# Kernel tuning notes

Hardware: AMD Instinct MI355X
Metric: run time of the kernel (lower is better)

## Reference

```python
import jax, jax.numpy as jnp
import numpy as np
from jax import lax

B, L, DIN, H = 16, 100, 6144, 1024
DI, N, DTR, K, NC = 2048, 16, 64, 4, 16  # d_inner, d_state, dt_rank, d_conv, num_classes


def setup_inputs() -> dict:
    key = jax.random.key(0)
    ks = jax.random.split(key, 10)
    def s(k, shape, sc=0.02):
        return jax.random.normal(k, shape, dtype=jnp.float32) * sc
    return dict(
        x=jax.random.normal(ks[0], (B, L, DIN), dtype=jnp.float32),
        W_in=s(ks[1], (DIN, H)), b_in=jnp.zeros((H,), jnp.float32),
        in_proj_w=s(ks[2], (H, 2 * DI)),
        conv_w=s(ks[3], (DI, K), 0.1), conv_b=jnp.zeros((DI,), jnp.float32),
        x_proj_w=s(ks[4], (DI, DTR + 2 * N)),
        dt_proj_w=s(ks[5], (DTR, DI), 0.1),
        dt_proj_b=jnp.full((DI,), float(np.log(np.expm1(0.01))), jnp.float32),
        A_log=jnp.log(jnp.broadcast_to(jnp.arange(1, N + 1, dtype=jnp.float32), (DI, N))),
        D=jnp.ones((DI,), jnp.float32),
        out_proj_w=s(ks[6], (DI, H)),
        W_out=s(ks[7], (H, NC)), b_out=jnp.zeros((NC,), jnp.float32),
    )


def reference(x, W_in, b_in, in_proj_w, conv_w, conv_b, x_proj_w,
              dt_proj_w, dt_proj_b, A_log, D, out_proj_w, W_out, b_out):
    # input projection: [B,L,DIN] -> [B,L,H]
    h = x @ W_in + b_in
    # Mamba block
    xz = h @ in_proj_w                      # [B,L,2*DI]
    xm, z = xz[..., :DI], xz[..., DI:]
    # depthwise causal conv1d, kernel K
    xp = jnp.pad(xm, ((0, 0), (K - 1, 0), (0, 0)))
    xc = sum(conv_w[:, k] * xp[:, k:k + L, :] for k in range(K)) + conv_b
    xc = jax.nn.silu(xc)                    # [B,L,DI]
    # input-dependent dt, B, C
    proj = xc @ x_proj_w                    # [B,L,DTR+2N]
    dt = proj[..., :DTR]
    Bm = proj[..., DTR:DTR + N]             # [B,L,N]
    Cm = proj[..., DTR + N:]                # [B,L,N]
    delta = jax.nn.softplus(dt @ dt_proj_w + dt_proj_b)  # [B,L,DI]
    A = -jnp.exp(A_log)                     # [DI,N]
    dA = jnp.exp(jnp.einsum('bld,dn->bldn', delta, A))          # [B,L,DI,N]
    dBx = (delta * xc)[..., None] * Bm[:, :, None, :]            # [B,L,DI,N]
    # selective scan over time: h_t = dA_t * h_{t-1} + dBx_t
    def step(hprev, inp):
        dA_t, dBx_t = inp
        hnew = dA_t * hprev + dBx_t
        return hnew, hnew
    h0 = jnp.zeros((xm.shape[0], DI, N), xm.dtype)
    _, hs = lax.scan(step, h0, (dA.transpose(1, 0, 2, 3), dBx.transpose(1, 0, 2, 3)))
    y = jnp.einsum('lbdn,bln->bld', hs, Cm)  # [B,L,DI]
    y = y + D * xc
    y = y * jax.nn.silu(z)
    out = y @ out_proj_w                     # [B,L,H]
    logits = out @ W_out + b_out             # [B,L,NC]
    return logits
```

## Files before the change

### kernel.cpp

```cpp
#include <hip/hip_runtime.h>
#include <hip/hip_bf16.h>
#include <stdint.h>

constexpr int Bb  = 16;
constexpr int Ll  = 100;
constexpr int DIN = 6144;
constexpr int Hh  = 1024;
constexpr int DI  = 2048;
constexpr int Nst = 16;
constexpr int DTR = 64;
constexpr int Kc  = 4;
constexpr int NC  = 16;
constexpr int M   = Bb * Ll;
constexpr int NCH = 4;
constexpr int CL  = Ll / NCH;

typedef __attribute__((ext_vector_type(8))) short short8;
typedef __attribute__((ext_vector_type(4))) float floatx4;

__device__ __forceinline__ float bf2f(unsigned short u) {
    union { uint32_t b; float f; } x; x.b = ((uint32_t)u) << 16; return x.f;
}
__device__ __forceinline__ unsigned short f2bf(float f) {
    union { float f; uint32_t b; } x; x.f = f;
    uint32_t r = x.b + 0x7FFF + ((x.b >> 16) & 1);
    return (unsigned short)(r >> 16);
}
__device__ __forceinline__ float fast_silu(float x) {
    return x / (1.f + __expf(-x));
}


template<bool SPLIT, bool BIAS, bool W16>
__global__ __launch_bounds__(512) void gemm_deep(
    const unsigned short* __restrict__ A, int lda,
    const unsigned short* __restrict__ Bt, int ldb,
    const float* __restrict__ bias,
    unsigned short* __restrict__ C16,
    unsigned short* __restrict__ Cpart,
    int Md, int Nd, int Kslab)
{
    __shared__ short As[3 * 256 * 64];
    __shared__ short Bs[3 * 128 * 64];

    const int nx = gridDim.x, ny = gridDim.y, nz = gridDim.z;
    const int nb = nx * ny * nz;
    int id = blockIdx.x + nx * (blockIdx.y + ny * blockIdx.z);
    int bx, by, bz;
    if ((nb & 7) == 0) {
        int swz = (id & 7) * (nb >> 3) + (id >> 3);
        bx = swz % nx;
        int rem = swz / nx;
        by = rem % ny;
        bz = rem / ny;
    } else {
        bx = blockIdx.x; by = blockIdx.y; bz = blockIdx.z;
    }

    const int tid  = threadIdx.x;
    const int lane = tid & 63;
    const int wid  = tid >> 6;
    const int wr   = wid >> 1;
    const int wc   = wid & 1;
    const int l15  = lane & 15;
    const int kg   = lane >> 4;
    const int gsw  = l15 & 7;
    const int m0   = bx * 256;
    const int n0   = by * 128;
    const int kbeg = SPLIT ? bz * Kslab : 0;

    floatx4 acc[4][4];
    #pragma unroll
    for (int m = 0; m < 4; m++)
        #pragma unroll
        for (int n = 0; n < 4; n++)
            acc[m][n] = (floatx4){0.f, 0.f, 0.f, 0.f};

    auto stage = [&](int buf, int k0) {
        #pragma unroll
        for (int j = 0; j < 4; j++) {
            int c = j * 512 + tid;
            int row = c >> 3, gl = c & 7;
            int gg = gl ^ (row & 7);
            int grow = m0 + row; grow = grow < Md ? grow : Md - 1;
            const __attribute__((address_space(1))) short* src =
                (const __attribute__((address_space(1))) short*)(A + (size_t)grow * lda + k0 + gg * 8);
            __builtin_amdgcn_global_load_lds(
                (const __attribute__((address_space(1))) void*)src,
                (__attribute__((address_space(3))) void*)&As[(buf * 2048 + c) * 8], 16, 0, 0);
        }
        #pragma unroll
        for (int j = 0; j < 2; j++) {
            int c = j * 512 + tid;
            int row = c >> 3, gl = c & 7;
            int gg = gl ^ (row & 7);
            int brow = n0 + row; brow = brow < Nd ? brow : Nd - 1;
            const __attribute__((address_space(1))) short* src =
                (const __attribute__((address_space(1))) short*)(Bt + (size_t)brow * ldb + k0 + gg * 8);
            __builtin_amdgcn_global_load_lds(
                (const __attribute__((address_space(1))) void*)src,
                (__attribute__((address_space(3))) void*)&Bs[(buf * 1024 + c) * 8], 16, 0, 0);
        }
    };

    const int nt = Kslab >> 6;
    stage(0, kbeg);
    stage(1, kbeg + 64);

    for (int t = 0; t < nt; t++) {
        const int cur = t % 3;
        if (t + 2 < nt) {
            stage((t + 2) % 3, kbeg + (t + 2) * 64);
            asm volatile("s_waitcnt vmcnt(12)" ::: "memory");
        } else if (t + 1 < nt) {
            asm volatile("s_waitcnt vmcnt(6)" ::: "memory");
        } else {
            asm volatile("s_waitcnt vmcnt(0)" ::: "memory");
        }
        __builtin_amdgcn_s_barrier();
        __builtin_amdgcn_sched_barrier(0);

        short8 a[2][4], bfr[2][4];
        #pragma unroll
        for (int kk = 0; kk < 2; kk++) {
            #pragma unroll
            for (int m = 0; m < 4; m++) {
                int row = wr * 64 + m * 16 + l15;
                int gs  = (kk * 4 + kg) ^ gsw;
                a[kk][m] = *(const short8*)&As[(cur * 2048 + row * 8 + gs) * 8];
            }
            #pragma unroll
            for (int n = 0; n < 4; n++) {
                int row = wc * 64 + n * 16 + l15;
                int gs  = (kk * 4 + kg) ^ gsw;
                bfr[kk][n] = *(const short8*)&Bs[(cur * 1024 + row * 8 + gs) * 8];
            }
        }
        __builtin_amdgcn_s_setprio(1);
        #pragma unroll
        for (int kk = 0; kk < 2; kk++)
            #pragma unroll
            for (int m = 0; m < 4; m++)
                #pragma unroll
                for (int n = 0; n < 4; n++)
                    acc[m][n] = __builtin_amdgcn_mfma_f32_16x16x32_bf16(a[kk][m], bfr[kk][n], acc[m][n], 0, 0, 0);
        __builtin_amdgcn_s_setprio(0);
        __builtin_amdgcn_sched_barrier(0);
        __builtin_amdgcn_s_barrier();
    }

    unsigned short* Cs = (unsigned short*)As;
    #pragma unroll
    for (int n = 0; n < 4; n++) {
        int col = wc * 64 + n * 16 + l15;
        float bv = BIAS ? bias[n0 + col] : 0.f;
        #pragma unroll
        for (int m = 0; m < 4; m++) {
            #pragma unroll
            for (int q = 0; q < 4; q++) {
                int row = wr * 64 + m * 16 + kg * 4 + q;
                Cs[row * 136 + col] = f2bf(acc[m][n][q] + bv);
            }
        }
    }
    __syncthreads();
    #pragma unroll
    for (int j = 0; j < 8; j++) {
        int c = j * 512 + tid;
        int row = c >> 4, cc = c & 15;
        int grow = m0 + row;
        if (grow >= Md) continue;
        short8 v = *(const short8*)&Cs[row * 136 + cc * 8];
        if (SPLIT)
            *(short8*)&Cpart[(size_t)bz * Md * Nd + (size_t)grow * Nd + n0 + cc * 8] = v;
        else if (W16)
            *(short8*)&C16[(size_t)grow * Nd + n0 + cc * 8] = v;
    }
}

template<bool SPLIT, bool PARTBF, bool BIAS, int ACT, bool W32, bool W16>
__global__ __launch_bounds__(256) void gemm_mfma(
    const unsigned short* __restrict__ A, int lda,
    const unsigned short* __restrict__ Bt, int ldb,
    const float* __restrict__ bias,
    float* __restrict__ C32,
    unsigned short* __restrict__ C16,
    void* __restrict__ Cpart,
    int Md, int Nd, int Kslab)
{
    __shared__ short As[2][128 * 64];
    __shared__ short Bs[2][128 * 64];

    const int nx = gridDim.x, ny = gridDim.y, nz = gridDim.z;
    const int nb = nx * ny * nz;
    int id = blockIdx.x + nx * (blockIdx.y + ny * blockIdx.z);
    int bx, by, bz;
    if ((nb & 7) == 0) {
        int swz = (id & 7) * (nb >> 3) + (id >> 3);
        bx = swz % nx;
        int rem = swz / nx;
        by = rem % ny;
        bz = rem / ny;
    } else {
        bx = blockIdx.x; by = blockIdx.y; bz = blockIdx.z;
    }

    const int tid  = threadIdx.x;
    const int lane = tid & 63;
    const int wid  = tid >> 6;
    const int wr   = wid >> 1;
    const int wc   = wid & 1;
    const int l15  = lane & 15;
    const int kg   = lane >> 4;
    const int gsw  = l15 & 7;
    const int m0   = bx * 128;
    const int n0   = by * 128;
    const int kbeg = SPLIT ? bz * Kslab : 0;

    floatx4 acc[4][4];
    #pragma unroll
    for (int m = 0; m < 4; m++)
        #pragma unroll
        for (int n = 0; n < 4; n++)
            acc[m][n] = (floatx4){0.f, 0.f, 0.f, 0.f};

    auto stage = [&](int buf, int k0) {
        #pragma unroll
        for (int j = 0; j < 4; j++) {
            int c = j * 256 + tid;
            int row = c >> 3, gl = c & 7;
            int gg = gl ^ (row & 7);
            int grow = m0 + row; grow = grow < Md ? grow : Md - 1;
            const __attribute__((address_space(1))) short* src =
                (const __attribute__((address_space(1))) short*)(A + (size_t)grow * lda + k0 + gg * 8);
            __builtin_amdgcn_global_load_lds(
                (const __attribute__((address_space(1))) void*)src,
                (__attribute__((address_space(3))) void*)&As[buf][c * 8], 16, 0, 0);
        }
        #pragma unroll
        for (int j = 0; j < 4; j++) {
            int c = j * 256 + tid;
            int row = c >> 3, gl = c & 7;
            int gg = gl ^ (row & 7);
            int brow = n0 + row; brow = brow < Nd ? brow : Nd - 1;
            const __attribute__((address_space(1))) short* src =
                (const __attribute__((address_space(1))) short*)(Bt + (size_t)brow * ldb + k0 + gg * 8);
            __builtin_amdgcn_global_load_lds(
                (const __attribute__((address_space(1))) void*)src,
                (__attribute__((address_space(3))) void*)&Bs[buf][c * 8], 16, 0, 0);
        }
    };

    stage(0, kbeg);
    asm volatile("s_waitcnt vmcnt(0)" ::: "memory");
    __builtin_amdgcn_s_barrier();
    __builtin_amdgcn_sched_barrier(0);

    const int nt = Kslab >> 6;
    for (int t = 0; t < nt; t++) {
        const int cur = t & 1;
        if (t + 1 < nt) {
            stage(cur ^ 1, kbeg + (t + 1) * 64);
            asm volatile("s_waitcnt vmcnt(8)" ::: "memory");
        } else {
            asm volatile("s_waitcnt vmcnt(0)" ::: "memory");
        }
        __builtin_amdgcn_s_barrier();
        __builtin_amdgcn_sched_barrier(0);

        short8 a[2][4], bfr[2][4];
        #pragma unroll
        for (int kk = 0; kk < 2; kk++) {
            #pragma unroll
            for (int m = 0; m < 4; m++) {
                int row = wr * 64 + m * 16 + l15;
                int gs  = (kk * 4 + kg) ^ gsw;
                a[kk][m] = *(const short8*)&As[cur][(row * 8 + gs) * 8];
            }
            #pragma unroll
            for (int n = 0; n < 4; n++) {
                int row = wc * 64 + n * 16 + l15;
                int gs  = (kk * 4 + kg) ^ gsw;
                bfr[kk][n] = *(const short8*)&Bs[cur][(row * 8 + gs) * 8];
            }
        }
        #pragma unroll
        for (int kk = 0; kk < 2; kk++)
            #pragma unroll
            for (int m = 0; m < 4; m++)
                #pragma unroll
                for (int n = 0; n < 4; n++)
                    acc[m][n] = __builtin_amdgcn_mfma_f32_16x16x32_bf16(a[kk][m], bfr[kk][n], acc[m][n], 0, 0, 0);

        __builtin_amdgcn_sched_barrier(0);
        __builtin_amdgcn_s_barrier();
    }

    if (SPLIT) {
        #pragma unroll
        for (int n = 0; n < 4; n++) {
            int col = n0 + wc * 64 + n * 16 + l15;
            if (col >= Nd) continue;
            #pragma unroll
            for (int m = 0; m < 4; m++)
                #pragma unroll
                for (int q = 0; q < 4; q++) {
                    int row = m0 + wr * 64 + m * 16 + kg * 4 + q;
                    if (row >= Md) continue;
                    size_t ix = (size_t)bz * Md * Nd + (size_t)row * Nd + col;
                    if (PARTBF) ((unsigned short*)Cpart)[ix] = f2bf(acc[m][n][q]);
                    else        ((float*)Cpart)[ix] = acc[m][n][q];
                }
        }
    } else {
        #pragma unroll
        for (int n = 0; n < 4; n++) {
            int col = n0 + wc * 64 + n * 16 + l15;
            if (col >= Nd) continue;
            float bv = BIAS ? bias[col] : 0.f;
            #pragma unroll
            for (int m = 0; m < 4; m++)
                #pragma unroll
                for (int q = 0; q < 4; q++) {
                    int row = m0 + wr * 64 + m * 16 + kg * 4 + q;
                    if (row >= Md) continue;
                    float v = acc[m][n][q] + bv;
                    if (ACT == 1) v = fmaxf(v, 0.f) + log1pf(expf(-fabsf(v)));
                    if (W32) C32[(size_t)row * Nd + col] = v;
                    if (W16) C16[(size_t)row * Nd + col] = f2bf(v);
                }
        }
    }
}

template<int S, bool BIAS, int ACT, bool W32, bool W16>
__global__ __launch_bounds__(256) void reduce_split(
    const float* __restrict__ P, const float* __restrict__ bias,
    float* __restrict__ C32, unsigned short* __restrict__ C16,
    int total, int nmask)
{
    int i = (blockIdx.x * 256 + threadIdx.x) * 4;
    float4 v = *(const float4*)&P[i];
    #pragma unroll
    for (int s = 1; s < S; s++) {
        float4 p = *(const float4*)&P[(size_t)s * total + i];
        v.x += p.x; v.y += p.y; v.z += p.z; v.w += p.w;
    }
    float r[4] = {v.x, v.y, v.z, v.w};
    #pragma unroll
    for (int j = 0; j < 4; j++) {
        float t = r[j];
        if (BIAS) t += bias[(i + j) & nmask];
        if (ACT == 1) t = fmaxf(t, 0.f) + log1pf(expf(-fabsf(t)));
        if (W32) C32[i + j] = t;
        if (W16) C16[i + j] = f2bf(t);
    }
}

template<int S, bool BIAS>
__global__ __launch_bounds__(256) void reduce_split_bf(
    const unsigned short* __restrict__ P, const float* __restrict__ bias,
    unsigned short* __restrict__ C16, int total, int nmask)
{
    int i = (blockIdx.x * 256 + threadIdx.x) * 8;
    float r[8] = {};
    #pragma unroll
    for (int s = 0; s < S; s++) {
        short8 p = *(const short8*)&P[(size_t)s * total + i];
        #pragma unroll
        for (int j = 0; j < 8; j++) r[j] += bf2f((unsigned short)p[j]);
    }
    short8 o;
    #pragma unroll
    for (int j = 0; j < 8; j++) {
        float t = r[j];
        if (BIAS) t += bias[(i + j) & nmask];
        o[j] = (short)f2bf(t);
    }
    *(short8*)&C16[i] = o;
}

__global__ __launch_bounds__(256) void f32_to_bf16_kernel(
    const float* __restrict__ in, unsigned short* __restrict__ out, int n4)
{
    int i = (blockIdx.x * 256 + threadIdx.x) * 4;
    float4 v = *(const float4*)&in[i];
    out[i + 0] = f2bf(v.x);
    out[i + 1] = f2bf(v.y);
    out[i + 2] = f2bf(v.z);
    out[i + 3] = f2bf(v.w);
}

__global__ __launch_bounds__(256) void transpose_f32_bf16(
    const float* __restrict__ in, unsigned short* __restrict__ out, int K, int N)
{
    __shared__ float t[32][33];
    int k0 = blockIdx.x * 32, n0 = blockIdx.y * 32;
    int tx = threadIdx.x & 31, ty = threadIdx.x >> 5;
    #pragma unroll
    for (int i = 0; i < 4; i++)
        t[ty + i * 8][tx] = in[(size_t)(k0 + ty + i * 8) * N + n0 + tx];
    __syncthreads();
    #pragma unroll
    for (int i = 0; i < 4; i++)
        out[(size_t)(n0 + ty + i * 8) * K + k0 + tx] = f2bf(t[tx][ty + i * 8]);
}

__global__ __launch_bounds__(256) void conv_silu_kernel(
    const unsigned short* __restrict__ xz, const float* __restrict__ conv_w,
    const float* __restrict__ conv_b, float* __restrict__ xc,
    unsigned short* __restrict__ xc_bf)
{
    int idx = blockIdx.x * 256 + threadIdx.x;
    if (idx >= Bb * Ll * DI) return;
    int d  = idx & (DI - 1);
    int bl = idx >> 11;
    int l  = bl % Ll;

    float acc = conv_b[d];
    #pragma unroll
    for (int k = 0; k < Kc; k++) {
        int ls = l + k - (Kc - 1);
        if (ls >= 0)
            acc = fmaf(conv_w[d * Kc + k], bf2f(xz[(size_t)(bl + ls - l) * (2 * DI) + d]), acc);
    }
    float s = fast_silu(acc);
    xc[idx] = s;
    xc_bf[idx] = f2bf(s);
}

__global__ __launch_bounds__(256) void scan_part1(
    const float* __restrict__ delta, const float* __restrict__ xc,
    const float* __restrict__ proj,  const float* __restrict__ A_log,
    float* __restrict__ Pbuf, float* __restrict__ Sbuf)
{
    const int t    = threadIdx.x;
    const int nq   = t & 3;
    const int dloc = t >> 2;
    const int d    = blockIdx.x * 64 + dloc;
    const int b    = blockIdx.y;
    const int c    = blockIdx.z;

    float4 Alq = *(const float4*)&A_log[(size_t)d * Nst + nq * 4];
    float Ar0 = -expf(Alq.x), Ar1 = -expf(Alq.y), Ar2 = -expf(Alq.z), Ar3 = -expf(Alq.w);

    float h0 = 0.f, h1 = 0.f, h2 = 0.f, h3 = 0.f;
    float sdl = 0.f;

    for (int l = c * CL; l < (c + 1) * CL; l++) {
        size_t bl = (size_t)b * Ll + l;
        float dl  = delta[bl * DI + d];
        float xcv = xc[bl * DI + d];
        float dx  = dl * xcv;
        float4 Bv = *(const float4*)&proj[bl * (DTR + 2 * Nst) + DTR + nq * 4];

        h0 = fmaf(__expf(dl * Ar0), h0, dx * Bv.x);
        h1 = fmaf(__expf(dl * Ar1), h1, dx * Bv.y);
        h2 = fmaf(__expf(dl * Ar2), h2, dx * Bv.z);
        h3 = fmaf(__expf(dl * Ar3), h3, dx * Bv.w);
        sdl += dl;
    }

    size_t o = (((size_t)c * Bb + b) * DI + d) * Nst + nq * 4;
    *(float4*)&Pbuf[o] = (float4){__expf(sdl * Ar0), __expf(sdl * Ar1),
                                  __expf(sdl * Ar2), __expf(sdl * Ar3)};
    *(float4*)&Sbuf[o] = (float4){h0, h1, h2, h3};
}

__global__ __launch_bounds__(256) void scan_part2(
    const float* __restrict__ delta, const float* __restrict__ xc,
    const unsigned short* __restrict__ xz, const float* __restrict__ proj,
    const float* __restrict__ A_log, const float* __restrict__ Dv,
    const float* __restrict__ Pbuf, const float* __restrict__ Sbuf,
    unsigned short* __restrict__ y)
{
    const int t    = threadIdx.x;
    const int nq   = t & 3;
    const int dloc = t >> 2;
    const int d    = blockIdx.x * 64 + dloc;
    const int b    = blockIdx.y;
    const int c    = blockIdx.z;

    float4 Alq = *(const float4*)&A_log[(size_t)d * Nst + nq * 4];
    float Ar0 = -expf(Alq.x), Ar1 = -expf(Alq.y), Ar2 = -expf(Alq.z), Ar3 = -expf(Alq.w);
    const float Dd = Dv[d];

    float h0 = 0.f, h1 = 0.f, h2 = 0.f, h3 = 0.f;
    for (int cc = 0; cc < c; cc++) {
        size_t o = (((size_t)cc * Bb + b) * DI + d) * Nst + nq * 4;
        float4 Pv = *(const float4*)&Pbuf[o];
        float4 Sv = *(const float4*)&Sbuf[o];
        h0 = fmaf(Pv.x, h0, Sv.x);
        h1 = fmaf(Pv.y, h1, Sv.y);
        h2 = fmaf(Pv.z, h2, Sv.z);
        h3 = fmaf(Pv.w, h3, Sv.w);
    }

    for (int l = c * CL; l < (c + 1) * CL; l++) {
        size_t bl = (size_t)b * Ll + l;
        float dl  = delta[bl * DI + d];
        float xcv = xc[bl * DI + d];
        float zv  = bf2f(xz[bl * (2 * DI) + DI + d]);
        float dx  = dl * xcv;
        const float* p = proj + bl * (DTR + 2 * Nst);
        float4 Bv = *(const float4*)&p[DTR + nq * 4];
        float4 Cv = *(const float4*)&p[DTR + Nst + nq * 4];

        h0 = fmaf(__expf(dl * Ar0), h0, dx * Bv.x);
        h1 = fmaf(__expf(dl * Ar1), h1, dx * Bv.y);
        h2 = fmaf(__expf(dl * Ar2), h2, dx * Bv.z);
        h3 = fmaf(__expf(dl * Ar3), h3, dx * Bv.w);

        float yac = h0 * Cv.x + h1 * Cv.y + h2 * Cv.z + h3 * Cv.w;
        yac += __shfl_xor(yac, 1);
        yac += __shfl_xor(yac, 2);

        if (nq == 0) {
            float yv = yac + Dd * xcv;
            yv *= fast_silu(zv);
            y[bl * DI + d] = f2bf(yv);
        }
    }
}

__global__ __launch_bounds__(256) void gemm_n16(
    const unsigned short* __restrict__ A, const float* __restrict__ W,
    const float* __restrict__ bias, float* __restrict__ C, int Kd)
{
    int m  = blockIdx.x;
    int t  = threadIdx.x;
    int c  = t & 15;
    int kg = t >> 4;
    const unsigned short* a = A + (size_t)m * Kd;

    float acc = 0.f;
    for (int k = kg; k < Kd; k += 16)
        acc = fmaf(bf2f(a[k]), W[k * NC + c], acc);

    __shared__ float red[256];
    red[t] = acc;
    __syncthreads();
    #pragma unroll
    for (int s = 128; s >= 16; s >>= 1) {
        if (t < s) red[t] += red[t + s];
        __syncthreads();
    }
    if (t < 16) C[(size_t)m * NC + t] = red[t] + bias[t];
}

extern "C" void kernel_launch(void* const* d_in, const int* in_sizes, int n_in,
                              void* d_out, int out_size, void* d_ws, size_t ws_size,
                              hipStream_t stream) {
    const float* x         = (const float*)d_in[0];
    const float* W_in      = (const float*)d_in[1];
    const float* b_in      = (const float*)d_in[2];
    const float* in_proj_w = (const float*)d_in[3];
    const float* conv_w    = (const float*)d_in[4];
    const float* conv_b    = (const float*)d_in[5];
    const float* x_proj_w  = (const float*)d_in[6];
    const float* dt_proj_w = (const float*)d_in[7];
    const float* dt_proj_b = (const float*)d_in[8];
    const float* A_log     = (const float*)d_in[9];
    const float* Dv        = (const float*)d_in[10];
    const float* out_proj  = (const float*)d_in[11];
    const float* W_out     = (const float*)d_in[12];
    const float* b_out     = (const float*)d_in[13];
    float* logits = (float*)d_out;

    char* base = (char*)d_ws;
    size_t off = 0;
    auto alloc = [&](size_t bytes) {
        char* p = base + off;
        off += (bytes + 255) & ~(size_t)255;
        return p;
    };
    unsigned short* x_bf    = (unsigned short*)alloc((size_t)M * DIN * 2);
    unsigned short* Wt_in   = (unsigned short*)alloc((size_t)Hh * DIN * 2);
    unsigned short* Wt_ip   = (unsigned short*)alloc((size_t)(2 * DI) * Hh * 2);
    unsigned short* Wt_op   = (unsigned short*)alloc((size_t)Hh * DI * 2);
    unsigned short* xpw_t   = (unsigned short*)alloc((size_t)96 * DI * 2);
    unsigned short* dtw_t   = (unsigned short*)alloc((size_t)DI * DTR * 2);
    unsigned short* h_bf    = (unsigned short*)alloc((size_t)M * Hh * 2);
    unsigned short* xz_bf   = (unsigned short*)alloc((size_t)M * 2 * DI * 2);
    float*          xc      = (float*)alloc((size_t)M * DI * 4);
    float*          delta   = (float*)alloc((size_t)M * DI * 4);
    unsigned short* xc_bf   = (unsigned short*)alloc((size_t)M * DI * 2);
    float*          proj_f  = (float*)alloc((size_t)M * 96 * 4);
    unsigned short* proj_bf = (unsigned short*)alloc((size_t)M * 96 * 2);
    unsigned short* y_bf    = (unsigned short*)alloc((size_t)M * DI * 2);
    unsigned short* out_bf  = (unsigned short*)alloc((size_t)M * Hh * 2);

    unsigned short* P14 = (unsigned short*)xc;
    float*          P8  = delta;
    float*          Pbuf = (float*)x_bf;
    float*          Sbuf = Pbuf + (size_t)(NCH - 1) * Bb * DI * Nst;

    dim3 blk(256), blk5(512);

    f32_to_bf16_kernel<<<dim3((M * DIN) / 1024), blk, 0, stream>>>(x, x_bf, M * DIN);
    transpose_f32_bf16<<<dim3(DIN / 32, Hh / 32), blk, 0, stream>>>(W_in, Wt_in, DIN, Hh);
    transpose_f32_bf16<<<dim3(Hh / 32, (2 * DI) / 32), blk, 0, stream>>>(in_proj_w, Wt_ip, Hh, 2 * DI);
    transpose_f32_bf16<<<dim3(DI / 32, Hh / 32), blk, 0, stream>>>(out_proj, Wt_op, DI, Hh);
    transpose_f32_bf16<<<dim3(DI / 32, 96 / 32), blk, 0, stream>>>(x_proj_w, xpw_t, DI, 96);
    transpose_f32_bf16<<<dim3(DTR / 32, DI / 32), blk, 0, stream>>>(dt_proj_w, dtw_t, DTR, DI);

    gemm_deep<true, false, false><<<dim3(7, Hh / 128, 4), blk5, 0, stream>>>(
        x_bf, DIN, Wt_in, DIN, nullptr, nullptr, P14, M, Hh, DIN / 4);
    reduce_split_bf<4, true><<<dim3((M * Hh) / 2048), blk, 0, stream>>>(
        P14, b_in, h_bf, M * Hh, Hh - 1);

    gemm_deep<false, false, true><<<dim3(7, (2 * DI) / 128, 1), blk5, 0, stream>>>(
        h_bf, Hh, Wt_ip, Hh, nullptr, xz_bf, nullptr, M, 2 * DI, Hh);

    conv_silu_kernel<<<dim3((Bb * Ll * DI) / 256), blk, 0, stream>>>(
        xz_bf, conv_w, conv_b, xc, xc_bf);

    gemm_mfma<true, false, false, 0, false, false><<<dim3(13, 1, 8), blk, 0, stream>>>(
        xc_bf, DI, xpw_t, DI, nullptr, nullptr, nullptr, P8, M, 96, DI / 8);
    reduce_split<8, false, 0, true, true><<<dim3((M * 96) / 1024), blk, 0, stream>>>(
        P8, nullptr, proj_f, proj_bf, M * 96, 0);

    gemm_mfma<false, false, true, 1, true, false><<<dim3(13, DI / 128, 1), blk, 0, stream>>>(
        proj_bf, 96, dtw_t, DTR, dt_proj_b, delta, nullptr, nullptr, M, DI, DTR);

    scan_part1<<<dim3(DI / 64, Bb, NCH - 1), blk, 0, stream>>>(
        delta, xc, proj_f, A_log, Pbuf, Sbuf);
    scan_part2<<<dim3(DI / 64, Bb, NCH), blk, 0, stream>>>(
        delta, xc, xz_bf, proj_f, A_log, Dv, Pbuf, Sbuf, y_bf);

    gemm_deep<true, false, false><<<dim3(7, Hh / 128, 4), blk5, 0, stream>>>(
        y_bf, DI, Wt_op, DI, nullptr, nullptr, P14, M, Hh, DI / 4);
    reduce_split_bf<4, false><<<dim3((M * Hh) / 2048), blk, 0, stream>>>(
        P14, nullptr, out_bf, M * Hh, 0);

    gemm_n16<<<dim3(M), blk, 0, stream>>>(out_bf, W_out, b_out, logits, Hh);
}
```

Measured before the change: 246.3 us.

## Fuse input conversion and weight transposes into one prep kernel; tweak GEMM barriers

Merges the fp32-to-bf16 conversion of x and the five weight transpose kernels into a single launch that dispatches by block index, removing five kernel launches and their tail gaps. It also moves the block barrier in gemm_deep to just after the LDS fragment loads, with an explicit lgkmcnt wait, so the MFMA work runs after the barrier. It adds s_setprio around the MFMA loop in gemm_mfma. The block-range partitioning is hard-coded to these problem sizes, and the barrier move changes how the LDS buffers are protected in the pipelined loop.

```diff
diff --git a/kernel.cpp b/kernel.cpp
--- a/kernel.cpp
+++ b/kernel.cpp
@@ -30,6 +30,44 @@
     return x / (1.f + __expf(-x));
 }
 
+__global__ __launch_bounds__(256) void prep_kernel(
+    const float* __restrict__ x, unsigned short* __restrict__ x_bf,
+    const float* __restrict__ W_in, unsigned short* __restrict__ Wt_in,
+    const float* __restrict__ W_ip, unsigned short* __restrict__ Wt_ip,
+    const float* __restrict__ W_op, unsigned short* __restrict__ Wt_op,
+    const float* __restrict__ xpw,  unsigned short* __restrict__ xpw_t,
+    const float* __restrict__ dtw,  unsigned short* __restrict__ dtw_t)
+{
+    __shared__ float t[32][33];
+    int b = blockIdx.x;
+
+    if (b < 9600) {
+        int i = (b * 256 + threadIdx.x) * 4;
+        float4 v = *(const float4*)&x[i];
+        x_bf[i + 0] = f2bf(v.x);
+        x_bf[i + 1] = f2bf(v.y);
+        x_bf[i + 2] = f2bf(v.z);
+        x_bf[i + 3] = f2bf(v.w);
+        return;
+    }
+    const float* in; unsigned short* out; int K, N, bid;
+    if      (b < 15744) { in = W_in; out = Wt_in; K = DIN; N = Hh;     bid = b - 9600;  }
+    else if (b < 19840) { in = W_ip; out = Wt_ip; K = Hh;  N = 2 * DI; bid = b - 15744; }
+    else if (b < 21888) { in = W_op; out = Wt_op; K = DI;  N = Hh;     bid = b - 19840; }
+    else if (b < 22080) { in = xpw;  out = xpw_t; K = DI;  N = 96;     bid = b - 21888; }
+    else                { in = dtw;  out = dtw_t; K = DTR; N = DI;     bid = b - 22080; }
+
+    int kx = bid % (K / 32), ny = bid / (K / 32);
+    int k0 = kx * 32, n0 = ny * 32;
+    int tx = threadIdx.x & 31, ty = threadIdx.x >> 5;
+    #pragma unroll
+    for (int i = 0; i < 4; i++)
+        t[ty + i * 8][tx] = in[(size_t)(k0 + ty + i * 8) * N + n0 + tx];
+    __syncthreads();
+    #pragma unroll
+    for (int i = 0; i < 4; i++)
+        out[(size_t)(n0 + ty + i * 8) * K + k0 + tx] = f2bf(t[tx][ty + i * 8]);
+}
 
 template<bool SPLIT, bool BIAS, bool W16>
 __global__ __launch_bounds__(512) void gemm_deep(
@@ -136,6 +174,11 @@
                 bfr[kk][n] = *(const short8*)&Bs[(cur * 1024 + row * 8 + gs) * 8];
             }
         }
+        asm volatile("s_waitcnt lgkmcnt(0)" ::: "memory");
+        __builtin_amdgcn_sched_barrier(0);
+        __builtin_amdgcn_s_barrier();
+        __builtin_amdgcn_sched_barrier(0);
+
         __builtin_amdgcn_s_setprio(1);
         #pragma unroll
         for (int kk = 0; kk < 2; kk++)
@@ -145,8 +188,6 @@
                 for (int n = 0; n < 4; n++)
                     acc[m][n] = __builtin_amdgcn_mfma_f32_16x16x32_bf16(a[kk][m], bfr[kk][n], acc[m][n], 0, 0, 0);
         __builtin_amdgcn_s_setprio(0);
-        __builtin_amdgcn_sched_barrier(0);
-        __builtin_amdgcn_s_barrier();
     }
 
     unsigned short* Cs = (unsigned short*)As;
@@ -284,6 +325,7 @@
                 bfr[kk][n] = *(const short8*)&Bs[cur][(row * 8 + gs) * 8];
             }
         }
+        __builtin_amdgcn_s_setprio(1);
         #pragma unroll
         for (int kk = 0; kk < 2; kk++)
             #pragma unroll
@@ -291,7 +333,7 @@
                 #pragma unroll
                 for (int n = 0; n < 4; n++)
                     acc[m][n] = __builtin_amdgcn_mfma_f32_16x16x32_bf16(a[kk][m], bfr[kk][n], acc[m][n], 0, 0, 0);
-
+        __builtin_amdgcn_s_setprio(0);
         __builtin_amdgcn_sched_barrier(0);
         __builtin_amdgcn_s_barrier();
     }
@@ -378,32 +420,6 @@
         o[j] = (short)f2bf(t);
     }
     *(short8*)&C16[i] = o;
-}
-
-__global__ __launch_bounds__(256) void f32_to_bf16_kernel(
-    const float* __restrict__ in, unsigned short* __restrict__ out, int n4)
-{
-    int i = (blockIdx.x * 256 + threadIdx.x) * 4;
-    float4 v = *(const float4*)&in[i];
-    out[i + 0] = f2bf(v.x);
-    out[i + 1] = f2bf(v.y);
-    out[i + 2] = f2bf(v.z);
-    out[i + 3] = f2bf(v.w);
-}
-
-__global__ __launch_bounds__(256) void transpose_f32_bf16(
-    const float* __restrict__ in, unsigned short* __restrict__ out, int K, int N)
-{
-    __shared__ float t[32][33];
-    int k0 = blockIdx.x * 32, n0 = blockIdx.y * 32;
-    int tx = threadIdx.x & 31, ty = threadIdx.x >> 5;
-    #pragma unroll
-    for (int i = 0; i < 4; i++)
-        t[ty + i * 8][tx] = in[(size_t)(k0 + ty + i * 8) * N + n0 + tx];
-    __syncthreads();
-    #pragma unroll
-    for (int i = 0; i < 4; i++)
-        out[(size_t)(n0 + ty + i * 8) * K + k0 + tx] = f2bf(t[tx][ty + i * 8]);
 }
 
 __global__ __launch_bounds__(256) void conv_silu_kernel(
@@ -597,12 +613,9 @@
 
     dim3 blk(256), blk5(512);
 
-    f32_to_bf16_kernel<<<dim3((M * DIN) / 1024), blk, 0, stream>>>(x, x_bf, M * DIN);
-    transpose_f32_bf16<<<dim3(DIN / 32, Hh / 32), blk, 0, stream>>>(W_in, Wt_in, DIN, Hh);
-    transpose_f32_bf16<<<dim3(Hh / 32, (2 * DI) / 32), blk, 0, stream>>>(in_proj_w, Wt_ip, Hh, 2 * DI);
-    transpose_f32_bf16<<<dim3(DI / 32, Hh / 32), blk, 0, stream>>>(out_proj, Wt_op, DI, Hh);
-    transpose_f32_bf16<<<dim3(DI / 32, 96 / 32), blk, 0, stream>>>(x_proj_w, xpw_t, DI, 96);
-    transpose_f32_bf16<<<dim3(DTR / 32, DI / 32), blk, 0, stream>>>(dt_proj_w, dtw_t, DTR, DI);
+    prep_kernel<<<dim3(22208), blk, 0, stream>>>(
+        x, x_bf, W_in, Wt_in, in_proj_w, Wt_ip, out_proj, Wt_op,
+        x_proj_w, xpw_t, dt_proj_w, dtw_t);
 
     gemm_deep<true, false, false><<<dim3(7, Hh / 128, 4), blk5, 0, stream>>>(
         x_bf, DIN, Wt_in, DIN, nullptr, nullptr, P14, M, Hh, DIN / 4);
```

New measurement: 235.6 us (median of 2 runs). 4.3% less time.
